# Kernel optimization log

Measured on AMD Instinct MI355X. Metric: run time of the kernel, lower is better.

Reference implementation:

```python
import jax, jax.numpy as jnp
import numpy as np

B, N, D = 64, 256, 1024      # batch, n_patches (DINOv2 ViT-L/14 @224), feature dim
P, C = 2000, 200             # num_prototypes, num_classes (10 per class)
EPS = 1e-4


def setup_inputs() -> dict:
    key = jax.random.key(0)
    k1, k2 = jax.random.split(key)
    patches = jax.random.normal(k1, (B, N, D), dtype=jnp.float32)
    prototypes = jax.random.uniform(k2, (P, D), dtype=jnp.float32)  # torch.rand init
    # fc init: +1 for the prototype's own class, -0.5 elsewhere (_fc_init)
    per_class = P // C
    cls = jnp.arange(P) // per_class                     # [P]
    pos = jax.nn.one_hot(cls, C, dtype=jnp.float32)      # [P, C]
    fc_w = (1.0 * pos + (-0.5) * (1.0 - pos)).T          # [C, P]
    return {"patches": patches, "prototypes": prototypes, "fc_w": fc_w}


def reference(patches, prototypes, fc_w):
    x2 = jnp.sum(patches ** 2, axis=-1, keepdims=True)   # [B, N, 1] (== x2 @ ones.T broadcast)
    p2 = jnp.sum(prototypes ** 2, axis=-1)               # [P]
    xp = jnp.einsum('bnd,pd->bnp', patches, prototypes)  # [B, N, P]
    distances = jax.nn.relu(x2 - 2.0 * xp + p2[None, None, :])  # [B, N, P]
    # permute(0, 2, 1)
    attn_maps = jnp.transpose(distances, (0, 2, 1))       # [B, P, N]
    # -max_pool1d(-d, kernel=N) == min over patches
    min_distances = jnp.min(attn_maps, axis=-1)           # [B, P]
    # 'log' activation similarity
    prototype_activations = jnp.log((min_distances + 1.0) / (min_distances + EPS))
    logits = prototype_activations @ fc_w.T               # [B, C]
    return logits, attn_maps, min_distances
```

## Files before the change

kernel.cpp:

```cpp
#include <hip/hip_runtime.h>
#include <hip/hip_bf16.h>
#include <stdint.h>

#define B_   64
#define N_   256
#define D_   1024
#define P_   2000
#define C_   200
#define PP   2048
#define M_   (B_ * N_)
#define EPSA 1e-4f

using f32x4  = __attribute__((ext_vector_type(4))) float;
using bf16x8 = __attribute__((ext_vector_type(8))) short;

__device__ __forceinline__ unsigned short f2bf(float f) {
  uint32_t u = __builtin_bit_cast(uint32_t, f);
  uint32_t r = (u + 0x7FFFu + ((u >> 16) & 1u)) >> 16;
  return (unsigned short)r;
}

__global__ __launch_bounds__(256) void k_convert(
    const float* __restrict__ patches, const float* __restrict__ protos,
    unsigned short* __restrict__ pat_bf, unsigned short* __restrict__ pro_bf,
    float* __restrict__ x2, float* __restrict__ p2)
{
  const int row = blockIdx.x;
  const int t   = threadIdx.x;
  float4 v = make_float4(0.f, 0.f, 0.f, 0.f);
  if (row < M_) {
    v = *(const float4*)(patches + (size_t)row * D_ + t * 4);
  } else {
    const int p = row - M_;
    if (p < P_) v = *(const float4*)(protos + (size_t)p * D_ + t * 4);
  }
  ushort4 o;
  o.x = f2bf(v.x); o.y = f2bf(v.y); o.z = f2bf(v.z); o.w = f2bf(v.w);
  if (row < M_) *(ushort4*)(pat_bf + (size_t)row * D_ + t * 4) = o;
  else          *(ushort4*)(pro_bf + (size_t)(row - M_) * D_ + t * 4) = o;

  float s = v.x * v.x + v.y * v.y + v.z * v.z + v.w * v.w;
  #pragma unroll
  for (int off = 32; off >= 1; off >>= 1) s += __shfl_xor(s, off);
  __shared__ float sm[4];
  if ((t & 63) == 0) sm[t >> 6] = s;
  __syncthreads();
  if (t == 0) {
    const float tot = sm[0] + sm[1] + sm[2] + sm[3];
    if (row < M_) x2[row] = tot;
    else          p2[row - M_] = tot;
  }
}

__global__ __launch_bounds__(256) void k_gemm(
    const unsigned short* __restrict__ pro_bf,
    const unsigned short* __restrict__ pat_bf,
    const float* __restrict__ x2, const float* __restrict__ p2,
    float* __restrict__ attn)
{
  __shared__ unsigned short ldsA[128 * 64];
  __shared__ unsigned short ldsB[128 * 64];

  const int tid  = threadIdx.x;
  const int lane = tid & 63;
  const int wid  = tid >> 6;
  const int wp   = wid >> 1;
  const int wn   = wid & 1;
  const int m0   = blockIdx.x * 128;
  const int p0   = blockIdx.y * 128;

  f32x4 acc[4][4];
  #pragma unroll
  for (int i = 0; i < 4; i++)
    #pragma unroll
    for (int j = 0; j < 4; j++) acc[i][j] = (f32x4){0.f, 0.f, 0.f, 0.f};

  const int srowlane = lane >> 3;
  const int sslot    = lane & 7;

  for (int kt = 0; kt < D_ / 64; ++kt) {
    const unsigned short* gA = pro_bf + (size_t)p0 * D_ + kt * 64;
    const unsigned short* gB = pat_bf + (size_t)m0 * D_ + kt * 64;
    #pragma unroll
    for (int i = 0; i < 4; i++) {
      const int r  = wid * 32 + i * 8 + srowlane;
      const int sl = sslot ^ (r & 7);
      __builtin_amdgcn_global_load_lds(
          (const __attribute__((address_space(1))) void*)(gA + (size_t)r * D_ + sl * 8),
          (__attribute__((address_space(3))) void*)&ldsA[(wid * 32 + i * 8) * 64],
          16, 0, 0);
      __builtin_amdgcn_global_load_lds(
          (const __attribute__((address_space(1))) void*)(gB + (size_t)r * D_ + sl * 8),
          (__attribute__((address_space(3))) void*)&ldsB[(wid * 32 + i * 8) * 64],
          16, 0, 0);
    }
    __syncthreads();

    #pragma unroll
    for (int kk = 0; kk < 2; ++kk) {
      bf16x8 af[4], bfr[4];
      #pragma unroll
      for (int i = 0; i < 4; i++) {
        const int rA  = wp * 64 + i * 16 + (lane & 15);
        const int slA = (kk * 4 + (lane >> 4)) ^ (rA & 7);
        af[i] = *(const bf16x8*)&ldsA[rA * 64 + slA * 8];
        const int rB  = wn * 64 + i * 16 + (lane & 15);
        const int slB = (kk * 4 + (lane >> 4)) ^ (rB & 7);
        bfr[i] = *(const bf16x8*)&ldsB[rB * 64 + slB * 8];
      }
      #pragma unroll
      for (int i = 0; i < 4; i++)
        #pragma unroll
        for (int j = 0; j < 4; j++)
          acc[i][j] = __builtin_amdgcn_mfma_f32_16x16x32_bf16(
              af[i], bfr[j], acc[i][j], 0, 0, 0);
    }
    __syncthreads();
  }

  const int b = m0 >> 8;
  float* attn_b = attn + (size_t)b * (P_ * N_);
  float x2v[4]; int nn[4];
  #pragma unroll
  for (int j = 0; j < 4; j++) {
    const int m = m0 + wn * 64 + j * 16 + (lane & 15);
    x2v[j] = x2[m];
    nn[j]  = m & 255;
  }
  #pragma unroll
  for (int i = 0; i < 4; i++) {
    #pragma unroll
    for (int q = 0; q < 4; q++) {
      const int p = p0 + wp * 64 + i * 16 + (lane >> 4) * 4 + q;
      if (p < P_) {
        const float p2v = p2[p];
        float* rowp = attn_b + (size_t)p * N_;
        #pragma unroll
        for (int j = 0; j < 4; j++) {
          const float d = x2v[j] + p2v - 2.0f * acc[i][j][q];
          rowp[nn[j]] = fmaxf(d, 0.f);
        }
      }
    }
  }
}

__global__ __launch_bounds__(256) void k_min(
    const float* __restrict__ attn, float* __restrict__ min_out,
    float* __restrict__ act)
{
  const int gw   = (blockIdx.x * 256 + threadIdx.x) >> 6;
  const int lane = threadIdx.x & 63;
  const float4 v = ((const float4*)(attn + (size_t)gw * N_))[lane];
  float m = fminf(fminf(v.x, v.y), fminf(v.z, v.w));
  #pragma unroll
  for (int off = 32; off >= 1; off >>= 1) m = fminf(m, __shfl_xor(m, off));
  if (lane == 0) {
    min_out[gw] = m;
    act[gw] = logf((m + 1.0f) / (m + EPSA));
  }
}

__global__ __launch_bounds__(256) void k_logits(
    const float* __restrict__ act, const float* __restrict__ fc_w,
    float* __restrict__ out)
{
  const int gw   = (blockIdx.x * 256 + threadIdx.x) >> 6;
  const int lane = threadIdx.x & 63;
  const int b = gw & 63;
  const int c = gw >> 6;
  const float* a = act  + (size_t)b * P_;
  const float* w = fc_w + (size_t)c * P_;
  float s = 0.f;
  #pragma unroll
  for (int i = 0; i < 32; i++) {
    const int p = i * 64 + lane;
    if (p < P_) s += a[p] * w[p];
  }
  #pragma unroll
  for (int off = 32; off >= 1; off >>= 1) s += __shfl_xor(s, off);
  if (lane == 0) out[b * C_ + c] = s;
}

extern "C" void kernel_launch(void* const* d_in, const int* in_sizes, int n_in,
                              void* d_out, int out_size, void* d_ws, size_t ws_size,
                              hipStream_t stream)
{
  const float* patches = (const float*)d_in[0];
  const float* protos  = (const float*)d_in[1];
  const float* fc_w    = (const float*)d_in[2];

  float* out    = (float*)d_out;
  float* logits = out;
  float* attn   = out + (size_t)B_ * C_;
  float* minv   = out + (size_t)B_ * C_ + (size_t)B_ * P_ * N_;

  char* ws = (char*)d_ws;
  unsigned short* pat_bf = (unsigned short*)ws;  ws += (size_t)M_ * D_ * 2;
  unsigned short* pro_bf = (unsigned short*)ws;  ws += (size_t)PP * D_ * 2;
  float* x2  = (float*)ws;                       ws += (size_t)M_ * 4;
  float* p2  = (float*)ws;                       ws += (size_t)PP * 4;
  float* act = (float*)ws;

  hipLaunchKernelGGL(k_convert, dim3(M_ + PP), dim3(256), 0, stream,
                     patches, protos, pat_bf, pro_bf, x2, p2);
  hipLaunchKernelGGL(k_gemm, dim3(M_ / 128, PP / 128), dim3(256), 0, stream,
                     pro_bf, pat_bf, x2, p2, attn);
  hipLaunchKernelGGL(k_min, dim3((B_ * P_) / 4), dim3(256), 0, stream,
                     attn, minv, act);
  hipLaunchKernelGGL(k_logits, dim3((B_ * C_) / 4), dim3(256), 0, stream,
                     act, fc_w, logits);
}
```

Baseline: 289.1 us.

## Fuse min-reduction into 256x256 double-buffered GEMM with XCD-aware tile mapping

Replaces the 128x128 single-buffered GEMM with a 256x256 tile, 512-thread kernel that double-buffers its LDS tiles and overlaps the next tile's global-to-LDS loads with MFMA phases using explicit waitcnt and barriers. The per-prototype min over patches and the log activation are computed in the GEMM epilogue through a cross-wave LDS reduction, which removes the separate k_min pass that re-read the whole attention map. Work-groups are remapped so each XCD handles a contiguous set of batch tiles to improve L2 reuse. The manual wait counts and larger register footprint raise the risk of spills or ordering hazards.

```diff
diff --git a/kernel.cpp b/kernel.cpp
--- a/kernel.cpp
+++ b/kernel.cpp
@@ -11,6 +11,11 @@
 #define M_   (B_ * N_)
 #define EPSA 1e-4f
 
+#define BM   256
+#define BN   256
+#define BK   64
+#define NT   (D_ / BK)
+
 using f32x4  = __attribute__((ext_vector_type(4))) float;
 using bf16x8 = __attribute__((ext_vector_type(8))) short;
 
@@ -52,112 +57,164 @@
   }
 }
 
-__global__ __launch_bounds__(256) void k_gemm(
+#define VMW4 asm volatile("s_waitcnt vmcnt(4)" ::: "memory")
+#define VMW2 asm volatile("s_waitcnt vmcnt(2)" ::: "memory")
+#define VMW0 asm volatile("s_waitcnt vmcnt(0)" ::: "memory")
+#define NOPW ((void)0)
+#define BARR __builtin_amdgcn_s_barrier()
+
+#define STAGE(KT, H, NB) do {                                                  \
+  const int r0_ = ((H) >> 1) * 128;                                            \
+  const unsigned short* gb_ = (((H) & 1) == 0)                                 \
+      ? (pro_bf + (size_t)p0 * D_) : (pat_bf + (size_t)m0 * D_);               \
+  unsigned short* lb_ = ((((H) & 1) == 0) ? ldsA : ldsB) + (NB) * (BM * BK);   \
+  _Pragma("unroll")                                                            \
+  for (int i_ = 0; i_ < 2; ++i_) {                                             \
+    const int rr_  = r0_ + wid * 16 + i_ * 8;                                  \
+    const int row_ = rr_ + (lane >> 3);                                        \
+    const int sl_  = (lane & 7) ^ (row_ & 7);                                  \
+    __builtin_amdgcn_global_load_lds(                                          \
+      (const __attribute__((address_space(1))) void*)                          \
+          (gb_ + (size_t)row_ * D_ + (KT) * BK + sl_ * 8),                     \
+      (__attribute__((address_space(3))) void*)(lb_ + rr_ * BK), 16, 0, 0);    \
+  }                                                                            \
+} while (0)
+
+#define PHASE(PH, NH, DOSTAGE, VMWAIT, DOBAR) do {                             \
+  DOSTAGE;                                                                     \
+  bf16x8 af_[4][2], bq_[2][2];                                                 \
+  _Pragma("unroll")                                                            \
+  for (int i_ = 0; i_ < 4; ++i_)                                               \
+    _Pragma("unroll")                                                          \
+    for (int kk_ = 0; kk_ < 2; ++kk_) {                                        \
+      const int row_ = (PH) * 128 + wr * 64 + i_ * 16 + (lane & 15);           \
+      const int sl_  = (kk_ * 4 + (lane >> 4)) ^ (row_ & 7);                   \
+      af_[i_][kk_] = *(const bf16x8*)&ldsA[nb * (BM * BK) + row_ * BK + sl_ * 8];\
+    }                                                                          \
+  _Pragma("unroll")                                                            \
+  for (int j_ = 0; j_ < 2; ++j_)                                               \
+    _Pragma("unroll")                                                          \
+    for (int kk_ = 0; kk_ < 2; ++kk_) {                                        \
+      const int row_ = (NH) * 128 + wc * 32 + j_ * 16 + (lane & 15);           \
+      const int sl_  = (kk_ * 4 + (lane >> 4)) ^ (row_ & 7);                   \
+      bq_[j_][kk_] = *(const bf16x8*)&ldsB[nb * (BM * BK) + row_ * BK + sl_ * 8];\
+    }                                                                          \
+  __builtin_amdgcn_s_setprio(1);                                               \
+  _Pragma("unroll")                                                            \
+  for (int i_ = 0; i_ < 4; ++i_)                                               \
+    _Pragma("unroll")                                                          \
+    for (int j_ = 0; j_ < 2; ++j_)                                             \
+      _Pragma("unroll")                                                        \
+      for (int kk_ = 0; kk_ < 2; ++kk_)                                        \
+        acc[(PH) * 4 + i_][(NH) * 2 + j_] =                                    \
+            __builtin_amdgcn_mfma_f32_16x16x32_bf16(                           \
+                af_[i_][kk_], bq_[j_][kk_],                                    \
+                acc[(PH) * 4 + i_][(NH) * 2 + j_], 0, 0, 0);                   \
+  __builtin_amdgcn_s_setprio(0);                                               \
+  VMWAIT;                                                                      \
+  __builtin_amdgcn_sched_barrier(0);                                           \
+  DOBAR;                                                                       \
+  __builtin_amdgcn_sched_barrier(0);                                           \
+} while (0)
+
+__global__ __launch_bounds__(512, 2) void k_gemm(
     const unsigned short* __restrict__ pro_bf,
     const unsigned short* __restrict__ pat_bf,
     const float* __restrict__ x2, const float* __restrict__ p2,
-    float* __restrict__ attn)
-{
-  __shared__ unsigned short ldsA[128 * 64];
-  __shared__ unsigned short ldsB[128 * 64];
+    float* __restrict__ attn, float* __restrict__ minv, float* __restrict__ act)
+{
+  extern __shared__ unsigned short lds_u16[];
+  unsigned short* ldsA = lds_u16;
+  unsigned short* ldsB = lds_u16 + 2 * BM * BK;
+  float* wmin = (float*)lds_u16;
 
   const int tid  = threadIdx.x;
   const int lane = tid & 63;
   const int wid  = tid >> 6;
-  const int wp   = wid >> 1;
-  const int wn   = wid & 1;
-  const int m0   = blockIdx.x * 128;
-  const int p0   = blockIdx.y * 128;
-
-  f32x4 acc[4][4];
-  #pragma unroll
-  for (int i = 0; i < 4; i++)
+  const int wr   = wid >> 2;
+  const int wc   = wid & 3;
+
+  const int wg  = blockIdx.x;
+  const int xcd = wg & 7;
+  const int idx = wg >> 3;
+  const int mt  = xcd * 8 + (idx & 7);
+  const int pt  = idx >> 3;
+  const int b   = mt;
+  const int p0  = pt * BM;
+  const int m0  = mt * BN;
+
+  f32x4 acc[8][4];
+  #pragma unroll
+  for (int i = 0; i < 8; i++)
     #pragma unroll
     for (int j = 0; j < 4; j++) acc[i][j] = (f32x4){0.f, 0.f, 0.f, 0.f};
 
-  const int srowlane = lane >> 3;
-  const int sslot    = lane & 7;
-
-  for (int kt = 0; kt < D_ / 64; ++kt) {
-    const unsigned short* gA = pro_bf + (size_t)p0 * D_ + kt * 64;
-    const unsigned short* gB = pat_bf + (size_t)m0 * D_ + kt * 64;
+  STAGE(0, 0, 0); STAGE(0, 1, 0); STAGE(0, 2, 0); STAGE(0, 3, 0);
+  VMW4;
+  __builtin_amdgcn_sched_barrier(0);
+  BARR;
+  __builtin_amdgcn_sched_barrier(0);
+
+  int nb = 0;
+  #pragma unroll 1
+  for (int kt = 0; kt < NT - 1; ++kt) {
+    PHASE(0, 0, STAGE(kt + 1, 0, nb ^ 1), VMW4, BARR);
+    PHASE(1, 0, STAGE(kt + 1, 1, nb ^ 1), VMW4, BARR);
+    PHASE(1, 1, STAGE(kt + 1, 2, nb ^ 1), NOPW, BARR);
+    PHASE(0, 1, STAGE(kt + 1, 3, nb ^ 1), VMW4, BARR);
+    nb ^= 1;
+  }
+  PHASE(0, 0, NOPW, VMW2, BARR);
+  PHASE(1, 0, NOPW, VMW0, BARR);
+  PHASE(1, 1, NOPW, NOPW, NOPW);
+  PHASE(0, 1, NOPW, NOPW, NOPW);
+
+  __syncthreads();
+
+  float x2v[2][2]; int nn[2][2];
+  #pragma unroll
+  for (int nh = 0; nh < 2; ++nh)
     #pragma unroll
-    for (int i = 0; i < 4; i++) {
-      const int r  = wid * 32 + i * 8 + srowlane;
-      const int sl = sslot ^ (r & 7);
-      __builtin_amdgcn_global_load_lds(
-          (const __attribute__((address_space(1))) void*)(gA + (size_t)r * D_ + sl * 8),
-          (__attribute__((address_space(3))) void*)&ldsA[(wid * 32 + i * 8) * 64],
-          16, 0, 0);
-      __builtin_amdgcn_global_load_lds(
-          (const __attribute__((address_space(1))) void*)(gB + (size_t)r * D_ + sl * 8),
-          (__attribute__((address_space(3))) void*)&ldsB[(wid * 32 + i * 8) * 64],
-          16, 0, 0);
+    for (int j = 0; j < 2; ++j) {
+      const int nl = nh * 128 + wc * 32 + j * 16 + (lane & 15);
+      x2v[nh][j] = x2[m0 + nl];
+      nn[nh][j]  = nl;
     }
-    __syncthreads();
-
+  float* attn_b = attn + (size_t)b * (P_ * N_);
+
+  #pragma unroll
+  for (int pf = 0; pf < 8; ++pf) {
     #pragma unroll
-    for (int kk = 0; kk < 2; ++kk) {
-      bf16x8 af[4], bfr[4];
-      #pragma unroll
-      for (int i = 0; i < 4; i++) {
-        const int rA  = wp * 64 + i * 16 + (lane & 15);
-        const int slA = (kk * 4 + (lane >> 4)) ^ (rA & 7);
-        af[i] = *(const bf16x8*)&ldsA[rA * 64 + slA * 8];
-        const int rB  = wn * 64 + i * 16 + (lane & 15);
-        const int slB = (kk * 4 + (lane >> 4)) ^ (rB & 7);
-        bfr[i] = *(const bf16x8*)&ldsB[rB * 64 + slB * 8];
-      }
-      #pragma unroll
-      for (int i = 0; i < 4; i++)
-        #pragma unroll
-        for (int j = 0; j < 4; j++)
-          acc[i][j] = __builtin_amdgcn_mfma_f32_16x16x32_bf16(
-              af[i], bfr[j], acc[i][j], 0, 0, 0);
-    }
-    __syncthreads();
-  }
-
-  const int b = m0 >> 8;
-  float* attn_b = attn + (size_t)b * (P_ * N_);
-  float x2v[4]; int nn[4];
-  #pragma unroll
-  for (int j = 0; j < 4; j++) {
-    const int m = m0 + wn * 64 + j * 16 + (lane & 15);
-    x2v[j] = x2[m];
-    nn[j]  = m & 255;
-  }
-  #pragma unroll
-  for (int i = 0; i < 4; i++) {
-    #pragma unroll
-    for (int q = 0; q < 4; q++) {
-      const int p = p0 + wp * 64 + i * 16 + (lane >> 4) * 4 + q;
+    for (int q = 0; q < 4; ++q) {
+      const int pl = (pf >> 2) * 128 + wr * 64 + (pf & 3) * 16 + (lane >> 4) * 4 + q;
+      const int p  = p0 + pl;
+      float mn = 3.4e38f;
       if (p < P_) {
         const float p2v = p2[p];
         float* rowp = attn_b + (size_t)p * N_;
         #pragma unroll
-        for (int j = 0; j < 4; j++) {
-          const float d = x2v[j] + p2v - 2.0f * acc[i][j][q];
-          rowp[nn[j]] = fmaxf(d, 0.f);
-        }
+        for (int nh = 0; nh < 2; ++nh)
+          #pragma unroll
+          for (int j = 0; j < 2; ++j) {
+            const float d = fmaxf(x2v[nh][j] + p2v - 2.0f * acc[pf][nh * 2 + j][q], 0.f);
+            rowp[nn[nh][j]] = d;
+            mn = fminf(mn, d);
+          }
       }
+      #pragma unroll
+      for (int mask = 1; mask <= 8; mask <<= 1) mn = fminf(mn, __shfl_xor(mn, mask));
+      if ((lane & 15) == 0) wmin[wc * 256 + pl] = mn;
     }
   }
-}
-
-__global__ __launch_bounds__(256) void k_min(
-    const float* __restrict__ attn, float* __restrict__ min_out,
-    float* __restrict__ act)
-{
-  const int gw   = (blockIdx.x * 256 + threadIdx.x) >> 6;
-  const int lane = threadIdx.x & 63;
-  const float4 v = ((const float4*)(attn + (size_t)gw * N_))[lane];
-  float m = fminf(fminf(v.x, v.y), fminf(v.z, v.w));
-  #pragma unroll
-  for (int off = 32; off >= 1; off >>= 1) m = fminf(m, __shfl_xor(m, off));
-  if (lane == 0) {
-    min_out[gw] = m;
-    act[gw] = logf((m + 1.0f) / (m + EPSA));
+  __syncthreads();
+  if (tid < 256) {
+    const int p = p0 + tid;
+    if (p < P_) {
+      const float m = fminf(fminf(wmin[tid], wmin[256 + tid]),
+                            fminf(wmin[512 + tid], wmin[768 + tid]));
+      minv[b * P_ + p] = m;
+      act[b * P_ + p]  = logf((m + 1.0f) / (m + EPSA));
+    }
   }
 }
 
@@ -182,6 +239,8 @@
   if (lane == 0) out[b * C_ + c] = s;
 }
 
+#define GEMM_LDS_BYTES (4 * BM * BK * 2)
+
 extern "C" void kernel_launch(void* const* d_in, const int* in_sizes, int n_in,
                               void* d_out, int out_size, void* d_ws, size_t ws_size,
                               hipStream_t stream)
@@ -202,12 +261,15 @@
   float* p2  = (float*)ws;                       ws += (size_t)PP * 4;
   float* act = (float*)ws;
 
+  (void)hipFuncSetAttribute((const void*)k_gemm,
+                            hipFuncAttributeMaxDynamicSharedMemorySize,
+                            GEMM_LDS_BYTES);
+
   hipLaunchKernelGGL(k_convert, dim3(M_ + PP), dim3(256), 0, stream,
                      patches, protos, pat_bf, pro_bf, x2, p2);
-  hipLaunchKernelGGL(k_gemm, dim3(M_ / 128, PP / 128), dim3(256), 0, stream,
-                     pro_bf, pat_bf, x2, p2, attn);
-  hipLaunchKernelGGL(k_min, dim3((B_ * P_) / 4), dim3(256), 0, stream,
-                     attn, minv, act);
+  hipLaunchKernelGGL(k_gemm, dim3((M_ / BN) * (PP / BM)), dim3(512),
+                     GEMM_LDS_BYTES, stream,
+                     pro_bf, pat_bf, x2, p2, attn, minv, act);
   hipLaunchKernelGGL(k_logits, dim3((B_ * C_) / 4), dim3(256), 0, stream,
                      act, fc_w, logits);
 }
```

Result: faster. 263.5 us (-8.9%).
